# Optimization experiments

Measured on AMD Instinct MI355X. Metric: run time of the kernel, lower is better.

Reference implementation:

```python
import jax, jax.numpy as jnp
import numpy as np

B, N, C, O, K = 8, 1024, 64, 64, 3  # batch, nodes, in_c, out_c, Cheb order
EPS = 1e-12


def setup_inputs() -> dict:
    key = jax.random.key(0)
    ks = jax.random.split(key, 10)
    X_real = jax.random.normal(ks[0], (B, N, C), dtype=jnp.float32)
    X_imag = jax.random.normal(ks[1], (B, N, C), dtype=jnp.float32)
    L_real = jax.random.normal(ks[2], (B, K + 1, N, N), dtype=jnp.float32)
    L_imag = jax.random.normal(ks[3], (B, K + 1, N, N), dtype=jnp.float32)
    # Chebyshev weights: uniform(-stdv, stdv) then normalized to unit complex magnitude (as in __init__)
    stdv = 1.0 / np.sqrt(O)
    w_real = jax.random.uniform(ks[4], (K + 1, C, O), minval=-stdv, maxval=stdv, dtype=jnp.float32)
    w_imag = jax.random.uniform(ks[5], (K + 1, C, O), minval=-stdv, maxval=stdv, dtype=jnp.float32)
    mag = jnp.sqrt(w_real ** 2 + w_imag ** 2)
    w_real = w_real / mag
    w_imag = w_imag / mag
    # complex attention linear: maps 2*C -> 1
    a_stdv = 1.0 / np.sqrt(2 * C)
    attn_w_real = jax.random.uniform(ks[6], (2 * C,), minval=-a_stdv, maxval=a_stdv, dtype=jnp.float32)
    attn_w_imag = jax.random.uniform(ks[7], (2 * C,), minval=-a_stdv, maxval=a_stdv, dtype=jnp.float32)
    attn_b_real = jnp.zeros((1,), dtype=jnp.float32)
    attn_b_imag = jnp.zeros((1,), dtype=jnp.float32)
    # complex PReLU slopes (PyTorch PReLU default init 0.25)
    prelu_a_real = jnp.full((1,), 0.25, dtype=jnp.float32)
    prelu_a_imag = jnp.full((1,), 0.25, dtype=jnp.float32)
    return dict(X_real=X_real, X_imag=X_imag, L_real=L_real, L_imag=L_imag,
                w_real=w_real, w_imag=w_imag,
                attn_w_real=attn_w_real, attn_w_imag=attn_w_imag,
                attn_b_real=attn_b_real, attn_b_imag=attn_b_imag,
                prelu_a_real=prelu_a_real, prelu_a_imag=prelu_a_imag)


def reference(X_real, X_imag, L_real, L_imag, w_real, w_imag,
              attn_w_real, attn_w_imag, attn_b_real, attn_b_imag,
              prelu_a_real, prelu_a_imag):
    c = X_real.shape[-1]
    # --- attention scores: CVLinear on concat(x_i, x_j) decomposes into per-node terms ---
    Wr_i, Wr_j = attn_w_real[:c], attn_w_real[c:]
    Wi_i, Wi_j = attn_w_imag[:c], attn_w_imag[c:]
    sR_i = X_real @ Wr_i - X_imag @ Wi_i  # [B,N]
    sI_i = X_real @ Wi_i + X_imag @ Wr_i
    sR_j = X_real @ Wr_j - X_imag @ Wi_j
    sI_j = X_real @ Wi_j + X_imag @ Wr_j
    scores_r = sR_i[:, :, None] + sR_j[:, None, :] + attn_b_real  # [B,N,N]
    scores_i = sI_i[:, :, None] + sI_j[:, None, :] + attn_b_imag
    # --- complex PReLU (applied to real/imag separately) ---
    pr = jnp.where(scores_r >= 0, scores_r, prelu_a_real * scores_r)
    pi = jnp.where(scores_i >= 0, scores_i, prelu_a_imag * scores_i)
    # --- phase softmax over dim=1: softmax of magnitude, phase preserved ---
    mag = jnp.sqrt(pr ** 2 + pi ** 2)
    sm = jax.nn.softmax(mag, axis=1)
    scale = sm / (mag + EPS)
    ar = scale * pr  # [B,N,N] complex attention (real part)
    ai = scale * pi
    # --- modulate complex Laplacian stack [B,K+1,N,N] ---
    Lr = L_real * ar[:, None] - L_imag * ai[:, None]
    Li = L_real * ai[:, None] + L_imag * ar[:, None]
    # einsum 'bijk,bqjp->bijp' with q-size 1 == rowsum over k, then scale X per node j
    rowR = Lr.sum(-1)  # [B,K+1,N]
    rowI = Li.sum(-1)
    # complex (L-rowsum * X) @ W, summed over the K+1 terms (torch.sum dim=2 of stack)
    real = (jnp.einsum('bmj,bjc,mco->bjo', rowR, X_real, w_real)
            - jnp.einsum('bmj,bjc,mco->bjo', rowI, X_imag, w_imag))
    imag = (jnp.einsum('bmj,bjc,mco->bjo', rowI, X_real, w_real)
            + jnp.einsum('bmj,bjc,mco->bjo', rowR, X_imag, w_imag))
    return real, imag
```

## Files before the change

kernel.cpp:

```cpp
#include <hip/hip_runtime.h>

#define EPS_Q 1e-12f

typedef float nfloat4 __attribute__((ext_vector_type(4)));

__device__ __forceinline__ float wave_reduce_sum(float v) {
#pragma unroll
    for (int m = 32; m > 0; m >>= 1) v += __shfl_xor(v, m, 64);
    return v;
}

__global__ __launch_bounds__(256)
void k_scores(const float* __restrict__ Xr, const float* __restrict__ Xi,
              const float* __restrict__ awr, const float* __restrict__ awi,
              float* __restrict__ sRi, float* __restrict__ sIi,
              float4* __restrict__ aux) {
    const int lane = threadIdx.x & 63;
    const int row  = (blockIdx.x << 2) + (threadIdx.x >> 6);
    const float xr = Xr[row * 64 + lane];
    const float xi = Xi[row * 64 + lane];
    const float wri = awr[lane], wrj = awr[64 + lane];
    const float wii = awi[lane], wij = awi[64 + lane];
    float v0 = xr * wri - xi * wii;
    float v1 = xr * wii + xi * wri;
    float v2 = xr * wrj - xi * wij;
    float v3 = xr * wij + xi * wrj;
#pragma unroll
    for (int m = 32; m > 0; m >>= 1) {
        v0 += __shfl_xor(v0, m, 64);
        v1 += __shfl_xor(v1, m, 64);
        v2 += __shfl_xor(v2, m, 64);
        v3 += __shfl_xor(v3, m, 64);
    }
    if (lane == 0) {
        sRi[row] = v0;
        sIi[row] = v1;
        aux[row].x = v2;
        aux[row].y = v3;
    }
}

__global__ __launch_bounds__(256)
void k_softmax(const float* __restrict__ sRi, const float* __restrict__ sIi,
               float4* __restrict__ aux,
               const float* __restrict__ abr, const float* __restrict__ abi,
               const float* __restrict__ par_, const float* __restrict__ pai_) {
    const int lane = threadIdx.x & 63;
    const int row  = (blockIdx.x << 2) + (threadIdx.x >> 6);
    const int b    = row >> 10;
    const float br = abr[0], bi = abi[0], par = par_[0], pai = pai_[0];
    const float sRj = aux[row].x, sIj = aux[row].y;
    const float* pR = sRi + (b << 10);
    const float* pI = sIi + (b << 10);
    float mags[16];
    float mx = -3.4e38f;
#pragma unroll
    for (int t = 0; t < 16; ++t) {
        const int i = (t << 6) + lane;
        float sr = pR[i] + sRj + br;
        float si = pI[i] + sIj + bi;
        float pr = sr >= 0.f ? sr : par * sr;
        float pi = si >= 0.f ? si : pai * si;
        float mg = sqrtf(pr * pr + pi * pi);
        mags[t] = mg;
        mx = fmaxf(mx, mg);
    }
#pragma unroll
    for (int m = 32; m > 0; m >>= 1) mx = fmaxf(mx, __shfl_xor(mx, m, 64));
    float s = 0.f;
#pragma unroll
    for (int t = 0; t < 16; ++t) s += __expf(mags[t] - mx);
    s = wave_reduce_sum(s);
    if (lane == 0) {
        aux[row].z = mx;
        aux[row].w = 1.f / s;
    }
}

__global__ __launch_bounds__(256)
void k_rowreduce(const float* __restrict__ Lr, const float* __restrict__ Li,
                 const float* __restrict__ sRi, const float* __restrict__ sIi,
                 const float4* __restrict__ aux,
                 const float* __restrict__ abr, const float* __restrict__ abi,
                 const float* __restrict__ par_, const float* __restrict__ pai_,
                 float* __restrict__ rowR, float* __restrict__ rowI) {
    __shared__ __align__(16) float lar[2][1024];
    __shared__ __align__(16) float lai[2][1024];
    const int tid = threadIdx.x;
    const int b   = blockIdx.x >> 9;
    const int i0  = (blockIdx.x & 511) << 1;
    const float br = abr[0], bi = abi[0], par = par_[0], pai = pai_[0];
    const float sri0 = sRi[(b << 10) + i0],     sii0 = sIi[(b << 10) + i0];
    const float sri1 = sRi[(b << 10) + i0 + 1], sii1 = sIi[(b << 10) + i0 + 1];
    const float4* auxb = aux + (b << 10);

#pragma unroll
    for (int t = 0; t < 4; ++t) {
        const int j = (t << 8) + tid;
        const float4 ax = auxb[j];
        {
            float sr = sri0 + ax.x + br;
            float si = sii0 + ax.y + bi;
            float pr = sr >= 0.f ? sr : par * sr;
            float pi = si >= 0.f ? si : pai * si;
            float mg = sqrtf(pr * pr + pi * pi);
            float sc = __expf(mg - ax.z) * ax.w / (mg + EPS_Q);
            lar[0][j] = sc * pr;
            lai[0][j] = sc * pi;
        }
        {
            float sr = sri1 + ax.x + br;
            float si = sii1 + ax.y + bi;
            float pr = sr >= 0.f ? sr : par * sr;
            float pi = si >= 0.f ? si : pai * si;
            float mg = sqrtf(pr * pr + pi * pi);
            float sc = __expf(mg - ax.z) * ax.w / (mg + EPS_Q);
            lar[1][j] = sc * pr;
            lai[1][j] = sc * pi;
        }
    }
    __syncthreads();

    const int wave = tid >> 6, lane = tid & 63;
#pragma unroll
    for (int r = 0; r < 2; ++r) {
        const size_t base = ((size_t)((b * 4 + wave) * 1024 + (i0 + r))) * 1024;
        const nfloat4* LR = (const nfloat4*)(Lr + base);
        const nfloat4* LI = (const nfloat4*)(Li + base);
        const float4* AR = (const float4*)&lar[r][0];
        const float4* AI = (const float4*)&lai[r][0];
        float aR0 = 0.f, aI0 = 0.f, aR1 = 0.f, aI1 = 0.f;
#pragma unroll
        for (int t = 0; t < 4; ++t) {
            const int j4 = (t << 6) + lane;
            const nfloat4 lr = __builtin_nontemporal_load(&LR[j4]);
            const nfloat4 li = __builtin_nontemporal_load(&LI[j4]);
            const float4 a = AR[j4];
            const float4 c = AI[j4];
            aR0 += lr.x * a.x - li.x * c.x;  aI0 += lr.x * c.x + li.x * a.x;
            aR1 += lr.y * a.y - li.y * c.y;  aI1 += lr.y * c.y + li.y * a.y;
            aR0 += lr.z * a.z - li.z * c.z;  aI0 += lr.z * c.z + li.z * a.z;
            aR1 += lr.w * a.w - li.w * c.w;  aI1 += lr.w * c.w + li.w * a.w;
        }
        float aR = aR0 + aR1;
        float aI = aI0 + aI1;
#pragma unroll
        for (int m = 32; m > 0; m >>= 1) {
            aR += __shfl_xor(aR, m, 64);
            aI += __shfl_xor(aI, m, 64);
        }
        if (lane == 0) {
            rowR[((b << 2) + wave) * 1024 + i0 + r] = aR;
            rowI[((b << 2) + wave) * 1024 + i0 + r] = aI;
        }
    }
}

__global__ __launch_bounds__(256)
void k_output(const float* __restrict__ Xr, const float* __restrict__ Xi,
              const float* __restrict__ wr, const float* __restrict__ wi,
              const float* __restrict__ rowR, const float* __restrict__ rowI,
              float* __restrict__ out) {
    __shared__ float lxr[16][64];
    __shared__ float lxi[16][64];
    const int tid = threadIdx.x;
    const int rb  = blockIdx.x << 4;
    {
        const float4* s0 = (const float4*)(Xr + (size_t)rb * 64);
        const float4* s1 = (const float4*)(Xi + (size_t)rb * 64);
        ((float4*)&lxr[0][0])[tid] = s0[tid];
        ((float4*)&lxi[0][0])[tid] = s1[tid];
    }
    __syncthreads();
    const int wave = tid >> 6, lane = tid & 63;
    const int r0 = wave << 2;
    float u[4][4], v[4][4];
#pragma unroll
    for (int r = 0; r < 4; ++r)
#pragma unroll
        for (int m = 0; m < 4; ++m) { u[r][m] = 0.f; v[r][m] = 0.f; }
    for (int c = 0; c < 64; ++c) {
        float wrv[4], wiv[4];
#pragma unroll
        for (int m = 0; m < 4; ++m) {
            wrv[m] = wr[((m << 6) + c) * 64 + lane];
            wiv[m] = wi[((m << 6) + c) * 64 + lane];
        }
#pragma unroll
        for (int r = 0; r < 4; ++r) {
            const float xr = lxr[r0 + r][c];
            const float xi = lxi[r0 + r][c];
#pragma unroll
            for (int m = 0; m < 4; ++m) {
                u[r][m] += xr * wrv[m];
                v[r][m] += xi * wiv[m];
            }
        }
    }
#pragma unroll
    for (int r = 0; r < 4; ++r) {
        const int row = rb + r0 + r;
        const int b = row >> 10, j = row & 1023;
        float re = 0.f, im = 0.f;
#pragma unroll
        for (int m = 0; m < 4; ++m) {
            const float rr = rowR[(b << 12) + (m << 10) + j];
            const float ri = rowI[(b << 12) + (m << 10) + j];
            re += rr * u[r][m] - ri * v[r][m];
            im += ri * u[r][m] + rr * v[r][m];
        }
        out[(size_t)row * 64 + lane] = re;
        out[524288 + (size_t)row * 64 + lane] = im;
    }
}

extern "C" void kernel_launch(void* const* d_in, const int* in_sizes, int n_in,
                              void* d_out, int out_size, void* d_ws, size_t ws_size,
                              hipStream_t stream) {
    const float* Xr  = (const float*)d_in[0];
    const float* Xi  = (const float*)d_in[1];
    const float* Lr  = (const float*)d_in[2];
    const float* Li  = (const float*)d_in[3];
    const float* wr  = (const float*)d_in[4];
    const float* wi  = (const float*)d_in[5];
    const float* awr = (const float*)d_in[6];
    const float* awi = (const float*)d_in[7];
    const float* abr = (const float*)d_in[8];
    const float* abi = (const float*)d_in[9];
    const float* par = (const float*)d_in[10];
    const float* pai = (const float*)d_in[11];
    float* out = (float*)d_out;

    float*  ws   = (float*)d_ws;
    float*  sRi  = ws;
    float*  sIi  = ws + 8192;
    float4* aux  = (float4*)(ws + 16384);
    float*  rowR = ws + 49152;
    float*  rowI = ws + 81920;

    k_scores  <<<dim3(2048), dim3(256), 0, stream>>>(Xr, Xi, awr, awi, sRi, sIi, aux);
    k_softmax <<<dim3(2048), dim3(256), 0, stream>>>(sRi, sIi, aux, abr, abi, par, pai);
    k_rowreduce<<<dim3(4096), dim3(256), 0, stream>>>(Lr, Li, sRi, sIi, aux,
                                                      abr, abi, par, pai, rowR, rowI);
    k_output  <<<dim3(512),  dim3(256), 0, stream>>>(Xr, Xi, wr, wi, rowR, rowI, out);
}
```

Before: 323.8 us.

## Compute attention coefficients per wave in registers and reuse across all K+1 Laplacians

The row-reduce kernel now assigns one wave per (batch, row i). Each lane computes its 16 attention coefficients directly into registers and reuses them for all four Chebyshev orders, instead of staging two rows of coefficients in shared memory behind a block barrier. The packed float4 aux buffer is split into separate structure-of-arrays buffers so each lane can read them with vectorised loads. This removes the LDS traffic and the barrier, keeps more L loads in flight per wave, and cuts redundant coefficient work, at the cost of higher register pressure.

```diff
diff --git a/kernel.cpp b/kernel.cpp
--- a/kernel.cpp
+++ b/kernel.cpp
@@ -14,7 +14,7 @@
 void k_scores(const float* __restrict__ Xr, const float* __restrict__ Xi,
               const float* __restrict__ awr, const float* __restrict__ awi,
               float* __restrict__ sRi, float* __restrict__ sIi,
-              float4* __restrict__ aux) {
+              float* __restrict__ sRj, float* __restrict__ sIj) {
     const int lane = threadIdx.x & 63;
     const int row  = (blockIdx.x << 2) + (threadIdx.x >> 6);
     const float xr = Xr[row * 64 + lane];
@@ -35,21 +35,22 @@
     if (lane == 0) {
         sRi[row] = v0;
         sIi[row] = v1;
-        aux[row].x = v2;
-        aux[row].y = v3;
+        sRj[row] = v2;
+        sIj[row] = v3;
     }
 }
 
 __global__ __launch_bounds__(256)
 void k_softmax(const float* __restrict__ sRi, const float* __restrict__ sIi,
-               float4* __restrict__ aux,
+               const float* __restrict__ sRj, const float* __restrict__ sIj,
+               float* __restrict__ cmax, float* __restrict__ cinv,
                const float* __restrict__ abr, const float* __restrict__ abi,
                const float* __restrict__ par_, const float* __restrict__ pai_) {
     const int lane = threadIdx.x & 63;
     const int row  = (blockIdx.x << 2) + (threadIdx.x >> 6);
     const int b    = row >> 10;
     const float br = abr[0], bi = abi[0], par = par_[0], pai = pai_[0];
-    const float sRj = aux[row].x, sIj = aux[row].y;
+    const float sRjv = sRj[row], sIjv = sIj[row];
     const float* pR = sRi + (b << 10);
     const float* pI = sIi + (b << 10);
     float mags[16];
@@ -57,8 +58,8 @@
 #pragma unroll
     for (int t = 0; t < 16; ++t) {
         const int i = (t << 6) + lane;
-        float sr = pR[i] + sRj + br;
-        float si = pI[i] + sIj + bi;
+        float sr = pR[i] + sRjv + br;
+        float si = pI[i] + sIjv + bi;
         float pr = sr >= 0.f ? sr : par * sr;
         float pi = si >= 0.f ? si : pai * si;
         float mg = sqrtf(pr * pr + pi * pi);
@@ -72,86 +73,101 @@
     for (int t = 0; t < 16; ++t) s += __expf(mags[t] - mx);
     s = wave_reduce_sum(s);
     if (lane == 0) {
-        aux[row].z = mx;
-        aux[row].w = 1.f / s;
-    }
+        cmax[row] = mx;
+        cinv[row] = 1.f / s;
+    }
+}
+
+__device__ __forceinline__ void attn_coef(float srj, float sij, float mx, float is,
+                                          float sri, float sii,
+                                          float br, float bi, float par, float pai,
+                                          float& ar, float& ai) {
+    float sr = sri + srj + br;
+    float si = sii + sij + bi;
+    float pr = sr >= 0.f ? sr : par * sr;
+    float pi = si >= 0.f ? si : pai * si;
+    float mg = sqrtf(pr * pr + pi * pi);
+    float sc = __expf(mg - mx) * is / (mg + EPS_Q);
+    ar = sc * pr;
+    ai = sc * pi;
 }
 
 __global__ __launch_bounds__(256)
 void k_rowreduce(const float* __restrict__ Lr, const float* __restrict__ Li,
                  const float* __restrict__ sRi, const float* __restrict__ sIi,
-                 const float4* __restrict__ aux,
+                 const float* __restrict__ sRj, const float* __restrict__ sIj,
+                 const float* __restrict__ cmax, const float* __restrict__ cinv,
                  const float* __restrict__ abr, const float* __restrict__ abi,
                  const float* __restrict__ par_, const float* __restrict__ pai_,
                  float* __restrict__ rowR, float* __restrict__ rowI) {
-    __shared__ __align__(16) float lar[2][1024];
-    __shared__ __align__(16) float lai[2][1024];
-    const int tid = threadIdx.x;
-    const int b   = blockIdx.x >> 9;
-    const int i0  = (blockIdx.x & 511) << 1;
+    const int lane = threadIdx.x & 63;
+    const int wid  = (blockIdx.x << 2) + (threadIdx.x >> 6);
+    const int b    = wid >> 10;
+    const int i    = wid & 1023;
     const float br = abr[0], bi = abi[0], par = par_[0], pai = pai_[0];
-    const float sri0 = sRi[(b << 10) + i0],     sii0 = sIi[(b << 10) + i0];
-    const float sri1 = sRi[(b << 10) + i0 + 1], sii1 = sIi[(b << 10) + i0 + 1];
-    const float4* auxb = aux + (b << 10);
-
+    const float sri = sRi[wid], sii = sIi[wid];
+
+    const float4* SRJ = (const float4*)(sRj + (b << 10));
+    const float4* SIJ = (const float4*)(sIj + (b << 10));
+    const float4* CMX = (const float4*)(cmax + (b << 10));
+    const float4* CIV = (const float4*)(cinv + (b << 10));
+
+    float arv[16], aiv[16];
 #pragma unroll
     for (int t = 0; t < 4; ++t) {
-        const int j = (t << 8) + tid;
-        const float4 ax = auxb[j];
-        {
-            float sr = sri0 + ax.x + br;
-            float si = sii0 + ax.y + bi;
-            float pr = sr >= 0.f ? sr : par * sr;
-            float pi = si >= 0.f ? si : pai * si;
-            float mg = sqrtf(pr * pr + pi * pi);
-            float sc = __expf(mg - ax.z) * ax.w / (mg + EPS_Q);
-            lar[0][j] = sc * pr;
-            lai[0][j] = sc * pi;
-        }
-        {
-            float sr = sri1 + ax.x + br;
-            float si = sii1 + ax.y + bi;
-            float pr = sr >= 0.f ? sr : par * sr;
-            float pi = si >= 0.f ? si : pai * si;
-            float mg = sqrtf(pr * pr + pi * pi);
-            float sc = __expf(mg - ax.z) * ax.w / (mg + EPS_Q);
-            lar[1][j] = sc * pr;
-            lai[1][j] = sc * pi;
-        }
-    }
-    __syncthreads();
-
-    const int wave = tid >> 6, lane = tid & 63;
-#pragma unroll
-    for (int r = 0; r < 2; ++r) {
-        const size_t base = ((size_t)((b * 4 + wave) * 1024 + (i0 + r))) * 1024;
-        const nfloat4* LR = (const nfloat4*)(Lr + base);
-        const nfloat4* LI = (const nfloat4*)(Li + base);
-        const float4* AR = (const float4*)&lar[r][0];
-        const float4* AI = (const float4*)&lai[r][0];
-        float aR0 = 0.f, aI0 = 0.f, aR1 = 0.f, aI1 = 0.f;
+        const int j4 = (t << 6) + lane;
+        const float4 vr = SRJ[j4];
+        const float4 vi = SIJ[j4];
+        const float4 vm = CMX[j4];
+        const float4 vs = CIV[j4];
+        attn_coef(vr.x, vi.x, vm.x, vs.x, sri, sii, br, bi, par, pai,
+                  arv[(t << 2) + 0], aiv[(t << 2) + 0]);
+        attn_coef(vr.y, vi.y, vm.y, vs.y, sri, sii, br, bi, par, pai,
+                  arv[(t << 2) + 1], aiv[(t << 2) + 1]);
+        attn_coef(vr.z, vi.z, vm.z, vs.z, sri, sii, br, bi, par, pai,
+                  arv[(t << 2) + 2], aiv[(t << 2) + 2]);
+        attn_coef(vr.w, vi.w, vm.w, vs.w, sri, sii, br, bi, par, pai,
+                  arv[(t << 2) + 3], aiv[(t << 2) + 3]);
+    }
+
+    const size_t rb = ((size_t)b << 22) + ((size_t)i << 10);
+    const nfloat4* LR = (const nfloat4*)(Lr + rb);
+    const nfloat4* LI = (const nfloat4*)(Li + rb);
+
+    float accR[4] = {0.f, 0.f, 0.f, 0.f};
+    float accI[4] = {0.f, 0.f, 0.f, 0.f};
+#pragma unroll
+    for (int m = 0; m < 4; ++m) {
+        nfloat4 r[4], q[4];
 #pragma unroll
         for (int t = 0; t < 4; ++t) {
-            const int j4 = (t << 6) + lane;
-            const nfloat4 lr = __builtin_nontemporal_load(&LR[j4]);
-            const nfloat4 li = __builtin_nontemporal_load(&LI[j4]);
-            const float4 a = AR[j4];
-            const float4 c = AI[j4];
-            aR0 += lr.x * a.x - li.x * c.x;  aI0 += lr.x * c.x + li.x * a.x;
-            aR1 += lr.y * a.y - li.y * c.y;  aI1 += lr.y * c.y + li.y * a.y;
-            aR0 += lr.z * a.z - li.z * c.z;  aI0 += lr.z * c.z + li.z * a.z;
-            aR1 += lr.w * a.w - li.w * c.w;  aI1 += lr.w * c.w + li.w * a.w;
-        }
-        float aR = aR0 + aR1;
-        float aI = aI0 + aI1;
-#pragma unroll
-        for (int m = 32; m > 0; m >>= 1) {
-            aR += __shfl_xor(aR, m, 64);
-            aI += __shfl_xor(aI, m, 64);
+            r[t] = __builtin_nontemporal_load(&LR[(m << 18) + (t << 6) + lane]);
+            q[t] = __builtin_nontemporal_load(&LI[(m << 18) + (t << 6) + lane]);
+        }
+#pragma unroll
+        for (int t = 0; t < 4; ++t) {
+            accR[m] += r[t].x * arv[(t << 2) + 0] - q[t].x * aiv[(t << 2) + 0];
+            accI[m] += r[t].x * aiv[(t << 2) + 0] + q[t].x * arv[(t << 2) + 0];
+            accR[m] += r[t].y * arv[(t << 2) + 1] - q[t].y * aiv[(t << 2) + 1];
+            accI[m] += r[t].y * aiv[(t << 2) + 1] + q[t].y * arv[(t << 2) + 1];
+            accR[m] += r[t].z * arv[(t << 2) + 2] - q[t].z * aiv[(t << 2) + 2];
+            accI[m] += r[t].z * aiv[(t << 2) + 2] + q[t].z * arv[(t << 2) + 2];
+            accR[m] += r[t].w * arv[(t << 2) + 3] - q[t].w * aiv[(t << 2) + 3];
+            accI[m] += r[t].w * aiv[(t << 2) + 3] + q[t].w * arv[(t << 2) + 3];
+        }
+    }
+
+#pragma unroll
+    for (int m = 0; m < 4; ++m) {
+        float aR = accR[m], aI = accI[m];
+#pragma unroll
+        for (int s = 32; s > 0; s >>= 1) {
+            aR += __shfl_xor(aR, s, 64);
+            aI += __shfl_xor(aI, s, 64);
         }
         if (lane == 0) {
-            rowR[((b << 2) + wave) * 1024 + i0 + r] = aR;
-            rowI[((b << 2) + wave) * 1024 + i0 + r] = aI;
+            rowR[((b << 2) + m) * 1024 + i] = aR;
+            rowI[((b << 2) + m) * 1024 + i] = aI;
         }
     }
 }
@@ -231,16 +247,20 @@
     const float* pai = (const float*)d_in[11];
     float* out = (float*)d_out;
 
-    float*  ws   = (float*)d_ws;
-    float*  sRi  = ws;
-    float*  sIi  = ws + 8192;
-    float4* aux  = (float4*)(ws + 16384);
-    float*  rowR = ws + 49152;
-    float*  rowI = ws + 81920;
-
-    k_scores  <<<dim3(2048), dim3(256), 0, stream>>>(Xr, Xi, awr, awi, sRi, sIi, aux);
-    k_softmax <<<dim3(2048), dim3(256), 0, stream>>>(sRi, sIi, aux, abr, abi, par, pai);
-    k_rowreduce<<<dim3(4096), dim3(256), 0, stream>>>(Lr, Li, sRi, sIi, aux,
+    float* ws   = (float*)d_ws;
+    float* sRi  = ws;
+    float* sIi  = ws + 8192;
+    float* sRj  = ws + 16384;
+    float* sIj  = ws + 24576;
+    float* cmax = ws + 32768;
+    float* cinv = ws + 40960;
+    float* rowR = ws + 49152;
+    float* rowI = ws + 81920;
+
+    k_scores   <<<dim3(2048), dim3(256), 0, stream>>>(Xr, Xi, awr, awi, sRi, sIi, sRj, sIj);
+    k_softmax  <<<dim3(2048), dim3(256), 0, stream>>>(sRi, sIi, sRj, sIj, cmax, cinv,
+                                                      abr, abi, par, pai);
+    k_rowreduce<<<dim3(2048), dim3(256), 0, stream>>>(Lr, Li, sRi, sIi, sRj, sIj, cmax, cinv,
                                                       abr, abi, par, pai, rowR, rowI);
-    k_output  <<<dim3(512),  dim3(256), 0, stream>>>(Xr, Xi, wr, wi, rowR, rowI, out);
-}
+    k_output   <<<dim3(512),  dim3(256), 0, stream>>>(Xr, Xi, wr, wi, rowR, rowI, out);
+}
```

Result: no change. 320.3 us (-1.1%).
